# Performance work log

Hardware: AMD Instinct MI355X
Metric: run time of the kernel (lower is better)

## Reference

```python
import jax, jax.numpy as jnp
import numpy as np

# SMPL kinematic tree (24 joints); parent[0] = -1 (root)
PARENT = [-1, 0, 0, 0, 1, 2, 3, 4, 5, 6, 7, 8, 9, 9, 9, 12, 13, 14, 16, 17, 18, 19, 20, 21]
J = len(PARENT)  # 24


def _ancestor_matrix(parent):
    # A[j, k] = 1 if offset k contributes to joint j (k on path root->j, excluding root)
    n = len(parent)
    A = np.zeros((n, n), dtype=np.float32)
    for j in range(1, n):
        k = j
        while k > 0:
            A[j, k] = 1.0
            k = parent[k]
    return A

ANC = jnp.asarray(_ancestor_matrix(PARENT))  # [J, J]


def setup_inputs() -> dict:
    key = jax.random.key(0)
    k0, k1, k2 = jax.random.split(key, 3)
    B, D, H = 131072, 256, 512
    out_dim = (J - 1) * 4
    z = jax.random.normal(k0, (B, D), jnp.float32)
    W1 = jax.random.normal(k1, (D, H), jnp.float32) / np.float32(np.sqrt(D))
    b1 = jnp.zeros((H,), jnp.float32)
    W2 = jax.random.normal(k2, (H, out_dim), jnp.float32) / np.float32(np.sqrt(H))
    b2 = jnp.zeros((out_dim,), jnp.float32)
    return {"z": z, "W1": W1, "b1": b1, "W2": W2, "b2": b2}


def reference(z, W1, b1, W2, b2):
    B = z.shape[0]
    h = jax.nn.silu(z @ W1 + b1)                      # [B, 512]
    raw = (h @ W2 + b2).reshape(B, J - 1, 4)          # [B, J-1, 4]
    dir_raw = raw[..., :3]                            # [B, J-1, 3]
    len_raw = raw[..., 3]                             # [B, J-1]
    # F.normalize(dim=-1, eps=1e-6): x / max(||x||, eps)
    norm = jnp.linalg.norm(dir_raw, axis=-1, keepdims=True)
    direction = dir_raw / jnp.maximum(norm, 1e-6)
    length = jax.nn.softplus(len_raw)                 # [B, J-1]
    offset_non_root = direction * length[..., None]
    offsets = jnp.concatenate(
        [jnp.zeros((B, 1, 3), z.dtype), offset_non_root], axis=1
    )  # [B, J, 3]
    # Forward kinematics: joints[j] = sum of offsets along ancestor chain.
    # The sequential per-joint loop collapses to one matmul with the
    # precomputed ancestor incidence matrix (same math, depth-parallel).
    joints = jnp.einsum('jk,bkc->bjc', ANC, offsets)  # [B, J, 3]
    return (joints, offsets, length)
```

## Files before the change

kernel.cpp:

```cpp
#include <hip/hip_runtime.h>
#include <math.h>

typedef _Float16 half8 __attribute__((ext_vector_type(8)));
typedef float floatx4 __attribute__((ext_vector_type(4)));

#define DD 256
#define HH 512
#define OC 92
#define NJ 24
#define BM 64
#define NCHUNK 16
#define W2_OFF 131072
#define FLAG_OFF 180224
#define FCAP 16384
#define BUF_BYTES 16384

__constant__ int c_parent[NJ] = {-1,0,0,0,1,2,3,4,5,6,7,8,9,9,9,12,13,14,16,17,18,19,20,21};


__global__ __launch_bounds__(256)
void prep(const float* __restrict__ W1, const float* __restrict__ W2,
          _Float16* __restrict__ ws, int* __restrict__ flags) {
    int t = blockIdx.x * 256 + threadIdx.x;
    if (t == 0) flags[0] = 0;
    if (t < 16384) {
        int lane = t & 63;
        int cfrag = (t >> 6) & 1;
        int ks = (t >> 7) & 7;
        int ckI = t >> 10;
        int c = ckI * 32 + cfrag * 16 + (lane & 15);
        int kb = ks * 32 + 4 * (lane >> 4);
        half8 v;
        #pragma unroll
        for (int j = 0; j < 8; ++j) {
            int k = kb + (j & 3) + 16 * (j >> 2);
            v[j] = (_Float16)W1[k * HH + c];
        }
        *(half8*)(ws + t * 8) = v;
    } else if (t < 16384 + 6144) {
        int u = t - 16384;
        int lane = u & 63;
        int rest = u >> 6;
        int cfrag = rest % 6;
        int ckI = rest / 6;
        int c = cfrag * 16 + (lane & 15);
        int kb = ckI * 32 + 4 * (lane >> 4);
        half8 v;
        #pragma unroll
        for (int j = 0; j < 8; ++j) {
            int k = kb + (j & 3) + 16 * (j >> 2);
            v[j] = (c < OC) ? (_Float16)W2[k * OC + c] : (_Float16)0.0f;
        }
        *(half8*)(ws + W2_OFF + (ckI * 6 + cfrag) * 512 + lane * 8) = v;
    }
}

__global__ __launch_bounds__(256)
__attribute__((amdgpu_waves_per_eu(4)))
void fused_main(const float* __restrict__ z, const _Float16* __restrict__ wsp,
                const float* __restrict__ b1, const float* __restrict__ b2,
                float* __restrict__ out, long long Btot, int* __restrict__ flags)
{
    __shared__ __align__(16) char smem[35200];
    float* b1f = (float*)(smem + 32768);
    float* b2f = (float*)(smem + 34816);
    const int tid = threadIdx.x;
    const int w   = tid >> 6;
    const int l   = tid & 63;
    const int l15 = l & 15;
    const int l4  = l >> 4;

    const long long R0w = (long long)blockIdx.x * BM + w * 16;

#define STAGE(ck_, dstbuf_) do {                                                             \
    const char* s1g_ = (const char*)wsp + (size_t)(ck_) * 16384;                             \
    _Pragma("unroll")                                                                        \
    for (int i_ = 0; i_ < 4; ++i_) {                                                         \
        int g_ = w * 4 + i_;                                                                 \
        __builtin_amdgcn_global_load_lds(                                                    \
            (const __attribute__((address_space(1))) void*)(s1g_ + g_ * 1024 + l * 16),      \
            (__attribute__((address_space(3))) void*)((dstbuf_) + g_ * 1024), 16, 0, 0);     \
    }                                                                                        \
} while (0)

#define MF(a_, b_, c_) __builtin_amdgcn_mfma_f32_16x16x32_f16((a_), (b_), (c_), 0, 0, 0)

#define COMPUTE_CHUNK(bufc_, ck_) do {                                                       \
    const _Float16* s1_ = (const _Float16*)(bufc_);                                          \
    const _Float16* p2_ = wsp + W2_OFF + (ck_) * 3072 + l * 8;                               \
    half8 w2f_[6];                                                                           \
    _Pragma("unroll")                                                                        \
    for (int cf_ = 0; cf_ < 6; ++cf_) w2f_[cf_] = *(const half8*)(p2_ + cf_ * 512);          \
    floatx4 acc1_[2];                                                                        \
    acc1_[0] = (floatx4)0.0f; acc1_[1] = (floatx4)0.0f;                                      \
    _Pragma("unroll")                                                                        \
    for (int ks_ = 0; ks_ < 8; ++ks_) {                                                      \
        _Pragma("unroll")                                                                    \
        for (int cf_ = 0; cf_ < 2; ++cf_) {                                                  \
            half8 bh_ = *(const half8*)(s1_ + ((ks_ * 2 + cf_) * 64 + l) * 8);               \
            acc1_[cf_] = MF(bh_, zh[ks_], acc1_[cf_]);                                       \
        }                                                                                    \
    }                                                                                        \
    floatx4 vb1a_ = *(const floatx4*)(b1f + (ck_) * 32 + 4 * l4);                            \
    floatx4 vb1b_ = *(const floatx4*)(b1f + (ck_) * 32 + 16 + 4 * l4);                       \
    half8 ah_;                                                                               \
    _Pragma("unroll")                                                                        \
    for (int cf_ = 0; cf_ < 2; ++cf_) {                                                      \
        _Pragma("unroll")                                                                    \
        for (int i_ = 0; i_ < 4; ++i_) {                                                     \
            float a_ = acc1_[cf_][i_] + (cf_ ? vb1b_[i_] : vb1a_[i_]);                       \
            float hv_ = a_ * __builtin_amdgcn_rcpf(1.0f + __expf(-a_));                      \
            ah_[i_ | (cf_ << 2)] = (_Float16)hv_;                                            \
        }                                                                                    \
    }                                                                                        \
    _Pragma("unroll")                                                                        \
    for (int cf_ = 0; cf_ < 6; ++cf_) {                                                      \
        a2[cf_] = MF(w2f_[cf_], ah_, a2[cf_]);                                               \
    }                                                                                        \
} while (0)

    STAGE(0, smem);
    if (tid < 128) *(floatx4*)(b1f + tid * 4) = *(const floatx4*)(b1 + tid * 4);
    if (tid >= 128 && tid < 224) { int c = tid - 128; b2f[c] = (c < OC) ? b2[c] : 0.0f; }

    half8 zh[8];
    {
        const float* zrow = z + (R0w + l15) * DD;
        #pragma unroll
        for (int ks = 0; ks < 8; ++ks) {
            const float* p = zrow + ks * 32 + l4 * 4;
            floatx4 va = *(const floatx4*)p;
            floatx4 vb = *(const floatx4*)(p + 16);
            half8 th;
            th[0] = (_Float16)va[0]; th[1] = (_Float16)va[1];
            th[2] = (_Float16)va[2]; th[3] = (_Float16)va[3];
            th[4] = (_Float16)vb[0]; th[5] = (_Float16)vb[1];
            th[6] = (_Float16)vb[2]; th[7] = (_Float16)vb[3];
            zh[ks] = th;
        }
    }

    floatx4 a2[6];
    #pragma unroll
    for (int i = 0; i < 6; ++i) a2[i] = (floatx4)0.0f;

    __syncthreads();

    #pragma unroll 1
    for (int t = 0; t < 8; ++t) {
        STAGE(2 * t + 1, smem + BUF_BYTES);
        COMPUTE_CHUNK(smem, 2 * t);
        asm volatile("s_waitcnt vmcnt(0)" ::: "memory");
        __builtin_amdgcn_s_barrier();
        if (t < 7) STAGE(2 * t + 2, smem);
        COMPUTE_CHUNK(smem + BUF_BYTES, 2 * t + 1);
        asm volatile("s_waitcnt vmcnt(0)" ::: "memory");
        __builtin_amdgcn_s_barrier();
    }

    float* joints  = out;
    float* offsets = out + Btot * (NJ * 3);
    float* length  = out + 2 * Btot * (NJ * 3);

    {
        float* s_off = (float*)(smem + w * 6080);
        float* s_len = s_off + 1152;
        const int r = l15;
        #pragma unroll
        for (int cf = 0; cf < 6; ++cf) {
            const int j = 4 * cf + l4;
            if (j < NJ - 1) {
                float x  = a2[cf][0] + b2f[4 * j + 0];
                float y  = a2[cf][1] + b2f[4 * j + 1];
                float zz = a2[cf][2] + b2f[4 * j + 2];
                float lr = a2[cf][3] + b2f[4 * j + 3];
                float nrm = sqrtf(x * x + y * y + zz * zz);
                float inv = __builtin_amdgcn_rcpf(fmaxf(nrm, 1e-6f));
                float len = fmaxf(lr, 0.0f) + __logf(1.0f + __expf(-fabsf(lr)));
                if (len > 12.0f * nrm) {
                    int fi = atomicAdd(&flags[0], 1);
                    if (fi < FCAP) flags[1 + fi] = (int)(R0w + r);
                }
                s_off[r * 72 + 3 * (j + 1) + 0] = x * inv * len;
                s_off[r * 72 + 3 * (j + 1) + 1] = y * inv * len;
                s_off[r * 72 + 3 * (j + 1) + 2] = zz * inv * len;
                s_len[r * 23 + j] = len;
            }
        }
        if (l < 16) {
            s_off[l * 72 + 0] = 0.0f;
            s_off[l * 72 + 1] = 0.0f;
            s_off[l * 72 + 2] = 0.0f;
        }
        __syncthreads();

        {
            float* gdst = offsets + R0w * (NJ * 3);
            for (int t4 = l; t4 < 288; t4 += 64)
                *(float4*)(gdst + t4 * 4) = *(float4*)(s_off + t4 * 4);
        }
        {
            float* gdst = length + R0w * (NJ - 1);
            for (int t4 = l; t4 < 92; t4 += 64)
                *(float4*)(gdst + t4 * 4) = *(float4*)(s_len + t4 * 4);
        }
        for (int task = l; task < 16 * NJ; task += 64) {
            int rr = task / NJ;
            int j = task - rr * NJ;
            float jx = 0.0f, jy = 0.0f, jz = 0.0f;
            int k = j;
            while (k > 0) {
                jx += s_off[rr * 72 + 3 * k + 0];
                jy += s_off[rr * 72 + 3 * k + 1];
                jz += s_off[rr * 72 + 3 * k + 2];
                k = c_parent[k];
            }
            long long base = (R0w + rr) * (NJ * 3) + j * 3;
            joints[base + 0] = jx;
            joints[base + 1] = jy;
            joints[base + 2] = jz;
        }
    }
#undef STAGE
#undef COMPUTE_CHUNK
#undef MF
}

__global__ __launch_bounds__(256)
void fixup(const float* __restrict__ z, const float* __restrict__ W1,
           const float* __restrict__ b1, const float* __restrict__ W2,
           const float* __restrict__ b2, float* __restrict__ out,
           long long Btot, const int* __restrict__ flags)
{
    __shared__ float z_s[DD];
    __shared__ float h_s[HH];
    __shared__ float raw_s[96];
    __shared__ float off_s[72];
    int n = flags[0];
    if (n > FCAP) n = FCAP;
    if ((int)blockIdx.x >= n) return;
    const int tid = threadIdx.x;
    const long long row = flags[1 + blockIdx.x];

    float* joints  = out;
    float* offsets = out + Btot * (NJ * 3);
    float* length  = out + 2 * Btot * (NJ * 3);

    z_s[tid] = z[row * DD + tid];
    __syncthreads();
    for (int c = tid; c < HH; c += 256) {
        float acc = b1[c];
        for (int k = 0; k < DD; ++k) acc = fmaf(z_s[k], W1[k * HH + c], acc);
        h_s[c] = acc / (1.0f + expf(-acc));
    }
    __syncthreads();
    if (tid < OC) {
        float acc = b2[tid];
        for (int k = 0; k < HH; ++k) acc = fmaf(h_s[k], W2[k * OC + tid], acc);
        raw_s[tid] = acc;
    }
    __syncthreads();
    if (tid < NJ - 1) {
        int j = tid;
        float x  = raw_s[4 * j + 0];
        float y  = raw_s[4 * j + 1];
        float zz = raw_s[4 * j + 2];
        float lr = raw_s[4 * j + 3];
        float nrm = sqrtf(x * x + y * y + zz * zz);
        float inv = 1.0f / fmaxf(nrm, 1e-6f);
        float len = fmaxf(lr, 0.0f) + log1pf(expf(-fabsf(lr)));
        off_s[3 * (j + 1) + 0] = x * inv * len;
        off_s[3 * (j + 1) + 1] = y * inv * len;
        off_s[3 * (j + 1) + 2] = zz * inv * len;
        length[row * (NJ - 1) + j] = len;
    }
    if (tid < 3) off_s[tid] = 0.0f;
    __syncthreads();
    if (tid < NJ) {
        int j = tid;
        float jx = 0.0f, jy = 0.0f, jz = 0.0f;
        int k = j;
        while (k > 0) {
            jx += off_s[3 * k + 0];
            jy += off_s[3 * k + 1];
            jz += off_s[3 * k + 2];
            k = c_parent[k];
        }
        joints[row * (NJ * 3) + j * 3 + 0] = jx;
        joints[row * (NJ * 3) + j * 3 + 1] = jy;
        joints[row * (NJ * 3) + j * 3 + 2] = jz;
    }
    if (tid < NJ * 3) offsets[row * (NJ * 3) + tid] = off_s[tid];
}

extern "C" void kernel_launch(void* const* d_in, const int* in_sizes, int n_in,
                              void* d_out, int out_size, void* d_ws, size_t ws_size,
                              hipStream_t stream) {
    const float* z  = (const float*)d_in[0];
    const float* W1 = (const float*)d_in[1];
    const float* b1 = (const float*)d_in[2];
    const float* W2 = (const float*)d_in[3];
    const float* b2 = (const float*)d_in[4];
    float* out = (float*)d_out;
    _Float16* ws = (_Float16*)d_ws;
    int* flags = (int*)(ws + FLAG_OFF);

    const long long Btot = (long long)in_sizes[0] / DD;

    prep<<<88, 256, 0, stream>>>(W1, W2, ws, flags);
    fused_main<<<(int)(Btot / BM), 256, 0, stream>>>(z, ws, b1, b2, out, Btot, flags);
    fixup<<<4096, 256, 0, stream>>>(z, W1, b1, W2, b2, out, Btot, flags);
}
```

Before: 143.6 us.

## Triple-buffer W1 staging and prefetch W2 fragments one chunk ahead

Moves from double to triple buffering of the W1 chunks in LDS, so each stage is issued two chunks ahead and the barriers wait on partial vmcnt instead of draining all loads. W2 fragments are loaded into alternating register sets one chunk early, and sched_barriers pin the issue order. The goal is to hide global and LDS load latency behind the MFMA work. In exchange, LDS use per block rises to about 51 KB and the occupancy hint drops from 4 to 3 waves per EU. The hand-counted vmcnt values also make correctness fragile.

```diff
diff --git a/kernel.cpp b/kernel.cpp
--- a/kernel.cpp
+++ b/kernel.cpp
@@ -9,7 +9,6 @@
 #define OC 92
 #define NJ 24
 #define BM 64
-#define NCHUNK 16
 #define W2_OFF 131072
 #define FLAG_OFF 180224
 #define FCAP 16384
@@ -56,14 +55,14 @@
 }
 
 __global__ __launch_bounds__(256)
-__attribute__((amdgpu_waves_per_eu(4)))
+__attribute__((amdgpu_waves_per_eu(3)))
 void fused_main(const float* __restrict__ z, const _Float16* __restrict__ wsp,
                 const float* __restrict__ b1, const float* __restrict__ b2,
                 float* __restrict__ out, long long Btot, int* __restrict__ flags)
 {
-    __shared__ __align__(16) char smem[35200];
-    float* b1f = (float*)(smem + 32768);
-    float* b2f = (float*)(smem + 34816);
+    __shared__ __align__(16) char smem[51584];
+    float* b1f = (float*)(smem + 49152);
+    float* b2f = (float*)(smem + 51200);
     const int tid = threadIdx.x;
     const int w   = tid >> 6;
     const int l   = tid & 63;
@@ -72,25 +71,29 @@
 
     const long long R0w = (long long)blockIdx.x * BM + w * 16;
 
-#define STAGE(ck_, dstbuf_) do {                                                             \
+#define SBAR() __builtin_amdgcn_sched_barrier(0)
+
+#define STAGE(ck_, boff_) do {                                                               \
     const char* s1g_ = (const char*)wsp + (size_t)(ck_) * 16384;                             \
     _Pragma("unroll")                                                                        \
     for (int i_ = 0; i_ < 4; ++i_) {                                                         \
         int g_ = w * 4 + i_;                                                                 \
         __builtin_amdgcn_global_load_lds(                                                    \
             (const __attribute__((address_space(1))) void*)(s1g_ + g_ * 1024 + l * 16),      \
-            (__attribute__((address_space(3))) void*)((dstbuf_) + g_ * 1024), 16, 0, 0);     \
+            (__attribute__((address_space(3))) void*)(smem + (boff_) + g_ * 1024), 16, 0, 0);\
     }                                                                                        \
 } while (0)
 
+#define LOADW2(dst_, ck_) do {                                                               \
+    const _Float16* p2_ = wsp + W2_OFF + (ck_) * 3072 + l * 8;                               \
+    _Pragma("unroll")                                                                        \
+    for (int cf_ = 0; cf_ < 6; ++cf_) dst_[cf_] = *(const half8*)(p2_ + cf_ * 512);          \
+} while (0)
+
 #define MF(a_, b_, c_) __builtin_amdgcn_mfma_f32_16x16x32_f16((a_), (b_), (c_), 0, 0, 0)
 
-#define COMPUTE_CHUNK(bufc_, ck_) do {                                                       \
-    const _Float16* s1_ = (const _Float16*)(bufc_);                                          \
-    const _Float16* p2_ = wsp + W2_OFF + (ck_) * 3072 + l * 8;                               \
-    half8 w2f_[6];                                                                           \
-    _Pragma("unroll")                                                                        \
-    for (int cf_ = 0; cf_ < 6; ++cf_) w2f_[cf_] = *(const half8*)(p2_ + cf_ * 512);          \
+#define COMPUTE_CHUNK(boff_, ck_, w2f_) do {                                                 \
+    const _Float16* s1_ = (const _Float16*)(smem + (boff_));                                 \
     floatx4 acc1_[2];                                                                        \
     acc1_[0] = (floatx4)0.0f; acc1_[1] = (floatx4)0.0f;                                      \
     _Pragma("unroll")                                                                        \
@@ -119,9 +122,7 @@
     }                                                                                        \
 } while (0)
 
-    STAGE(0, smem);
-    if (tid < 128) *(floatx4*)(b1f + tid * 4) = *(const floatx4*)(b1 + tid * 4);
-    if (tid >= 128 && tid < 224) { int c = tid - 128; b2f[c] = (c < OC) ? b2[c] : 0.0f; }
+#define BOFF(c_) ((((c_) % 3)) * BUF_BYTES)
 
     half8 zh[8];
     {
@@ -139,28 +140,51 @@
             zh[ks] = th;
         }
     }
+    SBAR();
+    half8 w2fA[6], w2fB[6];
+    STAGE(0, 0);
+    SBAR();
+    LOADW2(w2fA, 0);
+    SBAR();
+    STAGE(1, BUF_BYTES);
+    SBAR();
+
+    if (tid < 128) *(floatx4*)(b1f + tid * 4) = *(const floatx4*)(b1 + tid * 4);
+    if (tid >= 128 && tid < 224) { int c = tid - 128; b2f[c] = (c < OC) ? b2[c] : 0.0f; }
 
     floatx4 a2[6];
     #pragma unroll
     for (int i = 0; i < 6; ++i) a2[i] = (floatx4)0.0f;
 
-    __syncthreads();
-
     #pragma unroll 1
-    for (int t = 0; t < 8; ++t) {
-        STAGE(2 * t + 1, smem + BUF_BYTES);
-        COMPUTE_CHUNK(smem, 2 * t);
-        asm volatile("s_waitcnt vmcnt(0)" ::: "memory");
+    for (int u = 0; u < 8; ++u) {
+        const int e = 2 * u, o = 2 * u + 1;
+        asm volatile("s_waitcnt vmcnt(4)" ::: "memory");
         __builtin_amdgcn_s_barrier();
-        if (t < 7) STAGE(2 * t + 2, smem);
-        COMPUTE_CHUNK(smem + BUF_BYTES, 2 * t + 1);
-        asm volatile("s_waitcnt vmcnt(0)" ::: "memory");
+        SBAR();
+        LOADW2(w2fB, o);
+        SBAR();
+        if (u < 7) STAGE(e + 2, BOFF(e + 2));
+        SBAR();
+        COMPUTE_CHUNK(BOFF(e), e, w2fA);
+        if (u < 7) { asm volatile("s_waitcnt vmcnt(4)" ::: "memory"); }
+        else       { asm volatile("s_waitcnt vmcnt(0)" ::: "memory"); }
         __builtin_amdgcn_s_barrier();
+        SBAR();
+        if (u < 7) {
+            LOADW2(w2fA, e + 2);
+            SBAR();
+            STAGE(o + 2, BOFF(o + 2));
+            SBAR();
+        }
+        COMPUTE_CHUNK(BOFF(o), o, w2fB);
     }
 
     float* joints  = out;
     float* offsets = out + Btot * (NJ * 3);
     float* length  = out + 2 * Btot * (NJ * 3);
+
+    __syncthreads();
 
     {
         float* s_off = (float*)(smem + w * 6080);
@@ -222,8 +246,11 @@
         }
     }
 #undef STAGE
+#undef LOADW2
 #undef COMPUTE_CHUNK
 #undef MF
+#undef BOFF
+#undef SBAR
 }
 
 __global__ __launch_bounds__(256)
```

New measurement: 152.6 us. 6.2% more time.

## Stage half of W1 into LDS per phase with 128-row, 512-thread blocks

Applied to the files above, without the earlier changes.

The main kernel now uses 512-thread blocks covering 128 rows and loads W1 in two 128 KB halves into LDS, instead of double-buffering 16 KB chunks with a barrier per chunk. This cuts the per-chunk barriers and doubles the rows that share each staged weight tile. The cost is one large LDS allocation per block (about 130 KB), which limits occupancy to one block per CU, and an exposed load stall at each half. The fixup kernel also changes to a grid-stride loop over 512 blocks instead of launching 4096 mostly idle blocks.

```diff
diff --git a/kernel.cpp b/kernel.cpp
--- a/kernel.cpp
+++ b/kernel.cpp
@@ -8,12 +8,10 @@
 #define HH 512
 #define OC 92
 #define NJ 24
-#define BM 64
-#define NCHUNK 16
+#define BM 128
 #define W2_OFF 131072
 #define FLAG_OFF 180224
 #define FCAP 16384
-#define BUF_BYTES 16384
 
 __constant__ int c_parent[NJ] = {-1,0,0,0,1,2,3,4,5,6,7,8,9,9,9,12,13,14,16,17,18,19,20,21};
 
@@ -55,15 +53,15 @@
     }
 }
 
-__global__ __launch_bounds__(256)
-__attribute__((amdgpu_waves_per_eu(4)))
+__global__ __launch_bounds__(512)
+__attribute__((amdgpu_waves_per_eu(2)))
 void fused_main(const float* __restrict__ z, const _Float16* __restrict__ wsp,
                 const float* __restrict__ b1, const float* __restrict__ b2,
                 float* __restrict__ out, long long Btot, int* __restrict__ flags)
 {
-    __shared__ __align__(16) char smem[35200];
-    float* b1f = (float*)(smem + 32768);
-    float* b2f = (float*)(smem + 34816);
+    __shared__ __align__(16) char smem[133504];
+    float* b1f = (float*)(smem + 131072);
+    float* b2f = (float*)(smem + 133120);
     const int tid = threadIdx.x;
     const int w   = tid >> 6;
     const int l   = tid & 63;
@@ -72,56 +70,18 @@
 
     const long long R0w = (long long)blockIdx.x * BM + w * 16;
 
-#define STAGE(ck_, dstbuf_) do {                                                             \
-    const char* s1g_ = (const char*)wsp + (size_t)(ck_) * 16384;                             \
+#define STAGEP(p_) do {                                                                      \
+    const char* sg_ = (const char*)wsp + (size_t)(p_) * 131072;                              \
     _Pragma("unroll")                                                                        \
-    for (int i_ = 0; i_ < 4; ++i_) {                                                         \
-        int g_ = w * 4 + i_;                                                                 \
+    for (int i_ = 0; i_ < 16; ++i_) {                                                        \
+        int g_ = w * 16 + i_;                                                                \
         __builtin_amdgcn_global_load_lds(                                                    \
-            (const __attribute__((address_space(1))) void*)(s1g_ + g_ * 1024 + l * 16),      \
-            (__attribute__((address_space(3))) void*)((dstbuf_) + g_ * 1024), 16, 0, 0);     \
+            (const __attribute__((address_space(1))) void*)(sg_ + g_ * 1024 + l * 16),       \
+            (__attribute__((address_space(3))) void*)(smem + g_ * 1024), 16, 0, 0);          \
     }                                                                                        \
 } while (0)
 
 #define MF(a_, b_, c_) __builtin_amdgcn_mfma_f32_16x16x32_f16((a_), (b_), (c_), 0, 0, 0)
-
-#define COMPUTE_CHUNK(bufc_, ck_) do {                                                       \
-    const _Float16* s1_ = (const _Float16*)(bufc_);                                          \
-    const _Float16* p2_ = wsp + W2_OFF + (ck_) * 3072 + l * 8;                               \
-    half8 w2f_[6];                                                                           \
-    _Pragma("unroll")                                                                        \
-    for (int cf_ = 0; cf_ < 6; ++cf_) w2f_[cf_] = *(const half8*)(p2_ + cf_ * 512);          \
-    floatx4 acc1_[2];                                                                        \
-    acc1_[0] = (floatx4)0.0f; acc1_[1] = (floatx4)0.0f;                                      \
-    _Pragma("unroll")                                                                        \
-    for (int ks_ = 0; ks_ < 8; ++ks_) {                                                      \
-        _Pragma("unroll")                                                                    \
-        for (int cf_ = 0; cf_ < 2; ++cf_) {                                                  \
-            half8 bh_ = *(const half8*)(s1_ + ((ks_ * 2 + cf_) * 64 + l) * 8);               \
-            acc1_[cf_] = MF(bh_, zh[ks_], acc1_[cf_]);                                       \
-        }                                                                                    \
-    }                                                                                        \
-    floatx4 vb1a_ = *(const floatx4*)(b1f + (ck_) * 32 + 4 * l4);                            \
-    floatx4 vb1b_ = *(const floatx4*)(b1f + (ck_) * 32 + 16 + 4 * l4);                       \
-    half8 ah_;                                                                               \
-    _Pragma("unroll")                                                                        \
-    for (int cf_ = 0; cf_ < 2; ++cf_) {                                                      \
-        _Pragma("unroll")                                                                    \
-        for (int i_ = 0; i_ < 4; ++i_) {                                                     \
-            float a_ = acc1_[cf_][i_] + (cf_ ? vb1b_[i_] : vb1a_[i_]);                       \
-            float hv_ = a_ * __builtin_amdgcn_rcpf(1.0f + __expf(-a_));                      \
-            ah_[i_ | (cf_ << 2)] = (_Float16)hv_;                                            \
-        }                                                                                    \
-    }                                                                                        \
-    _Pragma("unroll")                                                                        \
-    for (int cf_ = 0; cf_ < 6; ++cf_) {                                                      \
-        a2[cf_] = MF(w2f_[cf_], ah_, a2[cf_]);                                               \
-    }                                                                                        \
-} while (0)
-
-    STAGE(0, smem);
-    if (tid < 128) *(floatx4*)(b1f + tid * 4) = *(const floatx4*)(b1 + tid * 4);
-    if (tid >= 128 && tid < 224) { int c = tid - 128; b2f[c] = (c < OC) ? b2[c] : 0.0f; }
 
     half8 zh[8];
     {
@@ -140,27 +100,65 @@
         }
     }
 
+    STAGEP(0);
+    if (tid < 128) *(floatx4*)(b1f + tid * 4) = *(const floatx4*)(b1 + tid * 4);
+    if (tid >= 128 && tid < 224) { int c = tid - 128; b2f[c] = (c < OC) ? b2[c] : 0.0f; }
+
     floatx4 a2[6];
     #pragma unroll
     for (int i = 0; i < 6; ++i) a2[i] = (floatx4)0.0f;
 
+    asm volatile("s_waitcnt vmcnt(0)" ::: "memory");
     __syncthreads();
 
     #pragma unroll 1
-    for (int t = 0; t < 8; ++t) {
-        STAGE(2 * t + 1, smem + BUF_BYTES);
-        COMPUTE_CHUNK(smem, 2 * t);
-        asm volatile("s_waitcnt vmcnt(0)" ::: "memory");
-        __builtin_amdgcn_s_barrier();
-        if (t < 7) STAGE(2 * t + 2, smem);
-        COMPUTE_CHUNK(smem + BUF_BYTES, 2 * t + 1);
-        asm volatile("s_waitcnt vmcnt(0)" ::: "memory");
-        __builtin_amdgcn_s_barrier();
+    for (int p = 0; p < 2; ++p) {
+        for (int c = 0; c < 8; ++c) {
+            const int ck = p * 8 + c;
+            const _Float16* p2 = wsp + W2_OFF + ck * 3072 + l * 8;
+            half8 w2f[6];
+            #pragma unroll
+            for (int cf = 0; cf < 6; ++cf) w2f[cf] = *(const half8*)(p2 + cf * 512);
+
+            const _Float16* s1 = (const _Float16*)(smem + c * 16384);
+            floatx4 acc1[2];
+            acc1[0] = (floatx4)0.0f; acc1[1] = (floatx4)0.0f;
+            #pragma unroll
+            for (int ks = 0; ks < 8; ++ks) {
+                #pragma unroll
+                for (int cf = 0; cf < 2; ++cf) {
+                    half8 bh = *(const half8*)(s1 + ((ks * 2 + cf) * 64 + l) * 8);
+                    acc1[cf] = MF(bh, zh[ks], acc1[cf]);
+                }
+            }
+            floatx4 vb1a = *(const floatx4*)(b1f + ck * 32 + 4 * l4);
+            floatx4 vb1b = *(const floatx4*)(b1f + ck * 32 + 16 + 4 * l4);
+            half8 ah;
+            #pragma unroll
+            for (int cf = 0; cf < 2; ++cf) {
+                #pragma unroll
+                for (int i = 0; i < 4; ++i) {
+                    float a = acc1[cf][i] + (cf ? vb1b[i] : vb1a[i]);
+                    float hv = a * __builtin_amdgcn_rcpf(1.0f + __expf(-a));
+                    ah[i | (cf << 2)] = (_Float16)hv;
+                }
+            }
+            #pragma unroll
+            for (int cf = 0; cf < 6; ++cf) a2[cf] = MF(w2f[cf], ah, a2[cf]);
+        }
+        if (p == 0) {
+            __syncthreads();
+            STAGEP(1);
+            asm volatile("s_waitcnt vmcnt(0)" ::: "memory");
+            __syncthreads();
+        }
     }
 
     float* joints  = out;
     float* offsets = out + Btot * (NJ * 3);
     float* length  = out + 2 * Btot * (NJ * 3);
+
+    __syncthreads();
 
     {
         float* s_off = (float*)(smem + w * 6080);
@@ -221,8 +219,7 @@
             joints[base + 2] = jz;
         }
     }
-#undef STAGE
-#undef COMPUTE_CHUNK
+#undef STAGEP
 #undef MF
 }
 
@@ -238,59 +235,61 @@
     __shared__ float off_s[72];
     int n = flags[0];
     if (n > FCAP) n = FCAP;
-    if ((int)blockIdx.x >= n) return;
     const int tid = threadIdx.x;
-    const long long row = flags[1 + blockIdx.x];
 
     float* joints  = out;
     float* offsets = out + Btot * (NJ * 3);
     float* length  = out + 2 * Btot * (NJ * 3);
 
-    z_s[tid] = z[row * DD + tid];
-    __syncthreads();
-    for (int c = tid; c < HH; c += 256) {
-        float acc = b1[c];
-        for (int k = 0; k < DD; ++k) acc = fmaf(z_s[k], W1[k * HH + c], acc);
-        h_s[c] = acc / (1.0f + expf(-acc));
-    }
-    __syncthreads();
-    if (tid < OC) {
-        float acc = b2[tid];
-        for (int k = 0; k < HH; ++k) acc = fmaf(h_s[k], W2[k * OC + tid], acc);
-        raw_s[tid] = acc;
-    }
-    __syncthreads();
-    if (tid < NJ - 1) {
-        int j = tid;
-        float x  = raw_s[4 * j + 0];
-        float y  = raw_s[4 * j + 1];
-        float zz = raw_s[4 * j + 2];
-        float lr = raw_s[4 * j + 3];
-        float nrm = sqrtf(x * x + y * y + zz * zz);
-        float inv = 1.0f / fmaxf(nrm, 1e-6f);
-        float len = fmaxf(lr, 0.0f) + log1pf(expf(-fabsf(lr)));
-        off_s[3 * (j + 1) + 0] = x * inv * len;
-        off_s[3 * (j + 1) + 1] = y * inv * len;
-        off_s[3 * (j + 1) + 2] = zz * inv * len;
-        length[row * (NJ - 1) + j] = len;
-    }
-    if (tid < 3) off_s[tid] = 0.0f;
-    __syncthreads();
-    if (tid < NJ) {
-        int j = tid;
-        float jx = 0.0f, jy = 0.0f, jz = 0.0f;
-        int k = j;
-        while (k > 0) {
-            jx += off_s[3 * k + 0];
-            jy += off_s[3 * k + 1];
-            jz += off_s[3 * k + 2];
-            k = c_parent[k];
-        }
-        joints[row * (NJ * 3) + j * 3 + 0] = jx;
-        joints[row * (NJ * 3) + j * 3 + 1] = jy;
-        joints[row * (NJ * 3) + j * 3 + 2] = jz;
-    }
-    if (tid < NJ * 3) offsets[row * (NJ * 3) + tid] = off_s[tid];
+    for (int e = blockIdx.x; e < n; e += gridDim.x) {
+        const long long row = flags[1 + e];
+        __syncthreads();
+        z_s[tid] = z[row * DD + tid];
+        __syncthreads();
+        for (int c = tid; c < HH; c += 256) {
+            float acc = b1[c];
+            for (int k = 0; k < DD; ++k) acc = fmaf(z_s[k], W1[k * HH + c], acc);
+            h_s[c] = acc / (1.0f + expf(-acc));
+        }
+        __syncthreads();
+        if (tid < OC) {
+            float acc = b2[tid];
+            for (int k = 0; k < HH; ++k) acc = fmaf(h_s[k], W2[k * OC + tid], acc);
+            raw_s[tid] = acc;
+        }
+        __syncthreads();
+        if (tid < NJ - 1) {
+            int j = tid;
+            float x  = raw_s[4 * j + 0];
+            float y  = raw_s[4 * j + 1];
+            float zz = raw_s[4 * j + 2];
+            float lr = raw_s[4 * j + 3];
+            float nrm = sqrtf(x * x + y * y + zz * zz);
+            float inv = 1.0f / fmaxf(nrm, 1e-6f);
+            float len = fmaxf(lr, 0.0f) + log1pf(expf(-fabsf(lr)));
+            off_s[3 * (j + 1) + 0] = x * inv * len;
+            off_s[3 * (j + 1) + 1] = y * inv * len;
+            off_s[3 * (j + 1) + 2] = zz * inv * len;
+            length[row * (NJ - 1) + j] = len;
+        }
+        if (tid < 3) off_s[tid] = 0.0f;
+        __syncthreads();
+        if (tid < NJ) {
+            int j = tid;
+            float jx = 0.0f, jy = 0.0f, jz = 0.0f;
+            int k = j;
+            while (k > 0) {
+                jx += off_s[3 * k + 0];
+                jy += off_s[3 * k + 1];
+                jz += off_s[3 * k + 2];
+                k = c_parent[k];
+            }
+            joints[row * (NJ * 3) + j * 3 + 0] = jx;
+            joints[row * (NJ * 3) + j * 3 + 1] = jy;
+            joints[row * (NJ * 3) + j * 3 + 2] = jz;
+        }
+        if (tid < NJ * 3) offsets[row * (NJ * 3) + tid] = off_s[tid];
+    }
 }
 
 extern "C" void kernel_launch(void* const* d_in, const int* in_sizes, int n_in,
@@ -308,6 +307,6 @@
     const long long Btot = (long long)in_sizes[0] / DD;
 
     prep<<<88, 256, 0, stream>>>(W1, W2, ws, flags);
-    fused_main<<<(int)(Btot / BM), 256, 0, stream>>>(z, ws, b1, b2, out, Btot, flags);
-    fixup<<<4096, 256, 0, stream>>>(z, W1, b1, W2, b2, out, Btot, flags);
+    fused_main<<<(int)(Btot / BM), 512, 0, stream>>>(z, ws, b1, b2, out, Btot, flags);
+    fixup<<<512, 256, 0, stream>>>(z, W1, b1, W2, b2, out, Btot, flags);
 }
```

Result: slower. 203.9 us (+42.0%).

## Single-buffer W1 staging to raise occupancy; grid-stride fixup kernel

Applied to the files above, without the earlier changes.

Drops the double-buffered W1 chunk staging in LDS for a single 16KB buffer and raises the waves-per-EU hint from 4 to 8. The lower LDS and register budget per block is meant to let more blocks share a CU. The epilogue now runs in two passes of two waves each so the per-wave offset scratch fits in the smaller LDS. The fixup kernel becomes a grid-stride loop over 512 blocks instead of launching 4096 blocks that mostly exit early. The cost is that chunk loads no longer overlap with compute inside a block, and the tighter register cap may cause spills.

```diff
diff --git a/kernel.cpp b/kernel.cpp
--- a/kernel.cpp
+++ b/kernel.cpp
@@ -9,11 +9,9 @@
 #define OC 92
 #define NJ 24
 #define BM 64
-#define NCHUNK 16
 #define W2_OFF 131072
 #define FLAG_OFF 180224
 #define FCAP 16384
-#define BUF_BYTES 16384
 
 __constant__ int c_parent[NJ] = {-1,0,0,0,1,2,3,4,5,6,7,8,9,9,9,12,13,14,16,17,18,19,20,21};
 
@@ -56,14 +54,14 @@
 }
 
 __global__ __launch_bounds__(256)
-__attribute__((amdgpu_waves_per_eu(4)))
+__attribute__((amdgpu_waves_per_eu(8)))
 void fused_main(const float* __restrict__ z, const _Float16* __restrict__ wsp,
                 const float* __restrict__ b1, const float* __restrict__ b2,
                 float* __restrict__ out, long long Btot, int* __restrict__ flags)
 {
-    __shared__ __align__(16) char smem[35200];
-    float* b1f = (float*)(smem + 32768);
-    float* b2f = (float*)(smem + 34816);
+    __shared__ __align__(16) char smem[18816];
+    float* b1f = (float*)(smem + 16384);
+    float* b2f = (float*)(smem + 18432);
     const int tid = threadIdx.x;
     const int w   = tid >> 6;
     const int l   = tid & 63;
@@ -72,21 +70,21 @@
 
     const long long R0w = (long long)blockIdx.x * BM + w * 16;
 
-#define STAGE(ck_, dstbuf_) do {                                                             \
+#define STAGE(ck_) do {                                                                      \
     const char* s1g_ = (const char*)wsp + (size_t)(ck_) * 16384;                             \
     _Pragma("unroll")                                                                        \
     for (int i_ = 0; i_ < 4; ++i_) {                                                         \
         int g_ = w * 4 + i_;                                                                 \
         __builtin_amdgcn_global_load_lds(                                                    \
             (const __attribute__((address_space(1))) void*)(s1g_ + g_ * 1024 + l * 16),      \
-            (__attribute__((address_space(3))) void*)((dstbuf_) + g_ * 1024), 16, 0, 0);     \
+            (__attribute__((address_space(3))) void*)(smem + g_ * 1024), 16, 0, 0);          \
     }                                                                                        \
 } while (0)
 
 #define MF(a_, b_, c_) __builtin_amdgcn_mfma_f32_16x16x32_f16((a_), (b_), (c_), 0, 0, 0)
 
-#define COMPUTE_CHUNK(bufc_, ck_) do {                                                       \
-    const _Float16* s1_ = (const _Float16*)(bufc_);                                          \
+#define COMPUTE_CHUNK(ck_) do {                                                              \
+    const _Float16* s1_ = (const _Float16*)(smem);                                           \
     const _Float16* p2_ = wsp + W2_OFF + (ck_) * 3072 + l * 8;                               \
     half8 w2f_[6];                                                                           \
     _Pragma("unroll")                                                                        \
@@ -118,10 +116,6 @@
         a2[cf_] = MF(w2f_[cf_], ah_, a2[cf_]);                                               \
     }                                                                                        \
 } while (0)
-
-    STAGE(0, smem);
-    if (tid < 128) *(floatx4*)(b1f + tid * 4) = *(const floatx4*)(b1 + tid * 4);
-    if (tid >= 128 && tid < 224) { int c = tid - 128; b2f[c] = (c < OC) ? b2[c] : 0.0f; }
 
     half8 zh[8];
     {
@@ -139,87 +133,92 @@
             zh[ks] = th;
         }
     }
+    STAGE(0);
+    if (tid < 128) *(floatx4*)(b1f + tid * 4) = *(const floatx4*)(b1 + tid * 4);
+    if (tid >= 128 && tid < 224) { int c = tid - 128; b2f[c] = (c < OC) ? b2[c] : 0.0f; }
 
     floatx4 a2[6];
     #pragma unroll
     for (int i = 0; i < 6; ++i) a2[i] = (floatx4)0.0f;
 
-    __syncthreads();
-
     #pragma unroll 1
-    for (int t = 0; t < 8; ++t) {
-        STAGE(2 * t + 1, smem + BUF_BYTES);
-        COMPUTE_CHUNK(smem, 2 * t);
+    for (int ck = 0; ck < 16; ++ck) {
         asm volatile("s_waitcnt vmcnt(0)" ::: "memory");
         __builtin_amdgcn_s_barrier();
-        if (t < 7) STAGE(2 * t + 2, smem);
-        COMPUTE_CHUNK(smem + BUF_BYTES, 2 * t + 1);
-        asm volatile("s_waitcnt vmcnt(0)" ::: "memory");
+        COMPUTE_CHUNK(ck);
         __builtin_amdgcn_s_barrier();
+        if (ck < 15) STAGE(ck + 1);
     }
 
     float* joints  = out;
     float* offsets = out + Btot * (NJ * 3);
     float* length  = out + 2 * Btot * (NJ * 3);
 
-    {
-        float* s_off = (float*)(smem + w * 6080);
-        float* s_len = s_off + 1152;
-        const int r = l15;
-        #pragma unroll
-        for (int cf = 0; cf < 6; ++cf) {
-            const int j = 4 * cf + l4;
-            if (j < NJ - 1) {
-                float x  = a2[cf][0] + b2f[4 * j + 0];
-                float y  = a2[cf][1] + b2f[4 * j + 1];
-                float zz = a2[cf][2] + b2f[4 * j + 2];
-                float lr = a2[cf][3] + b2f[4 * j + 3];
-                float nrm = sqrtf(x * x + y * y + zz * zz);
-                float inv = __builtin_amdgcn_rcpf(fmaxf(nrm, 1e-6f));
-                float len = fmaxf(lr, 0.0f) + __logf(1.0f + __expf(-fabsf(lr)));
-                if (len > 12.0f * nrm) {
-                    int fi = atomicAdd(&flags[0], 1);
-                    if (fi < FCAP) flags[1 + fi] = (int)(R0w + r);
+    #pragma unroll 1
+    for (int pass = 0; pass < 2; ++pass) {
+        if ((w >> 1) == pass) {
+            float* s_off = (float*)(smem + (w & 1) * 6080);
+            float* s_len = s_off + 1152;
+            const int r = l15;
+            #pragma unroll
+            for (int cf = 0; cf < 6; ++cf) {
+                const int j = 4 * cf + l4;
+                if (j < NJ - 1) {
+                    float x  = a2[cf][0] + b2f[4 * j + 0];
+                    float y  = a2[cf][1] + b2f[4 * j + 1];
+                    float zz = a2[cf][2] + b2f[4 * j + 2];
+                    float lr = a2[cf][3] + b2f[4 * j + 3];
+                    float nrm = sqrtf(x * x + y * y + zz * zz);
+                    float inv = __builtin_amdgcn_rcpf(fmaxf(nrm, 1e-6f));
+                    float len = fmaxf(lr, 0.0f) + __logf(1.0f + __expf(-fabsf(lr)));
+                    if (len > 12.0f * nrm) {
+                        int fi = atomicAdd(&flags[0], 1);
+                        if (fi < FCAP) flags[1 + fi] = (int)(R0w + r);
+                    }
+                    s_off[r * 72 + 3 * (j + 1) + 0] = x * inv * len;
+                    s_off[r * 72 + 3 * (j + 1) + 1] = y * inv * len;
+                    s_off[r * 72 + 3 * (j + 1) + 2] = zz * inv * len;
+                    s_len[r * 23 + j] = len;
                 }
-                s_off[r * 72 + 3 * (j + 1) + 0] = x * inv * len;
-                s_off[r * 72 + 3 * (j + 1) + 1] = y * inv * len;
-                s_off[r * 72 + 3 * (j + 1) + 2] = zz * inv * len;
-                s_len[r * 23 + j] = len;
-            }
-        }
-        if (l < 16) {
-            s_off[l * 72 + 0] = 0.0f;
-            s_off[l * 72 + 1] = 0.0f;
-            s_off[l * 72 + 2] = 0.0f;
-        }
-        __syncthreads();
-
-        {
-            float* gdst = offsets + R0w * (NJ * 3);
-            for (int t4 = l; t4 < 288; t4 += 64)
-                *(float4*)(gdst + t4 * 4) = *(float4*)(s_off + t4 * 4);
-        }
-        {
-            float* gdst = length + R0w * (NJ - 1);
-            for (int t4 = l; t4 < 92; t4 += 64)
-                *(float4*)(gdst + t4 * 4) = *(float4*)(s_len + t4 * 4);
-        }
-        for (int task = l; task < 16 * NJ; task += 64) {
-            int rr = task / NJ;
-            int j = task - rr * NJ;
-            float jx = 0.0f, jy = 0.0f, jz = 0.0f;
-            int k = j;
-            while (k > 0) {
-                jx += s_off[rr * 72 + 3 * k + 0];
-                jy += s_off[rr * 72 + 3 * k + 1];
-                jz += s_off[rr * 72 + 3 * k + 2];
-                k = c_parent[k];
-            }
-            long long base = (R0w + rr) * (NJ * 3) + j * 3;
-            joints[base + 0] = jx;
-            joints[base + 1] = jy;
-            joints[base + 2] = jz;
-        }
+            }
+            if (l < 16) {
+                s_off[l * 72 + 0] = 0.0f;
+                s_off[l * 72 + 1] = 0.0f;
+                s_off[l * 72 + 2] = 0.0f;
+            }
+        }
+        __syncthreads();
+        if ((w >> 1) == pass) {
+            float* s_off = (float*)(smem + (w & 1) * 6080);
+            float* s_len = s_off + 1152;
+            {
+                float* gdst = offsets + R0w * (NJ * 3);
+                for (int t4 = l; t4 < 288; t4 += 64)
+                    *(float4*)(gdst + t4 * 4) = *(float4*)(s_off + t4 * 4);
+            }
+            {
+                float* gdst = length + R0w * (NJ - 1);
+                for (int t4 = l; t4 < 92; t4 += 64)
+                    *(float4*)(gdst + t4 * 4) = *(float4*)(s_len + t4 * 4);
+            }
+            for (int task = l; task < 16 * NJ; task += 64) {
+                int rr = task / NJ;
+                int j = task - rr * NJ;
+                float jx = 0.0f, jy = 0.0f, jz = 0.0f;
+                int k = j;
+                while (k > 0) {
+                    jx += s_off[rr * 72 + 3 * k + 0];
+                    jy += s_off[rr * 72 + 3 * k + 1];
+                    jz += s_off[rr * 72 + 3 * k + 2];
+                    k = c_parent[k];
+                }
+                long long base = (R0w + rr) * (NJ * 3) + j * 3;
+                joints[base + 0] = jx;
+                joints[base + 1] = jy;
+                joints[base + 2] = jz;
+            }
+        }
+        if (pass == 0) __syncthreads();
     }
 #undef STAGE
 #undef COMPUTE_CHUNK
@@ -238,59 +237,61 @@
     __shared__ float off_s[72];
     int n = flags[0];
     if (n > FCAP) n = FCAP;
-    if ((int)blockIdx.x >= n) return;
     const int tid = threadIdx.x;
-    const long long row = flags[1 + blockIdx.x];
 
     float* joints  = out;
     float* offsets = out + Btot * (NJ * 3);
     float* length  = out + 2 * Btot * (NJ * 3);
 
-    z_s[tid] = z[row * DD + tid];
-    __syncthreads();
-    for (int c = tid; c < HH; c += 256) {
-        float acc = b1[c];
-        for (int k = 0; k < DD; ++k) acc = fmaf(z_s[k], W1[k * HH + c], acc);
-        h_s[c] = acc / (1.0f + expf(-acc));
-    }
-    __syncthreads();
-    if (tid < OC) {
-        float acc = b2[tid];
-        for (int k = 0; k < HH; ++k) acc = fmaf(h_s[k], W2[k * OC + tid], acc);
-        raw_s[tid] = acc;
-    }
-    __syncthreads();
-    if (tid < NJ - 1) {
-        int j = tid;
-        float x  = raw_s[4 * j + 0];
-        float y  = raw_s[4 * j + 1];
-        float zz = raw_s[4 * j + 2];
-        float lr = raw_s[4 * j + 3];
-        float nrm = sqrtf(x * x + y * y + zz * zz);
-        float inv = 1.0f / fmaxf(nrm, 1e-6f);
-        float len = fmaxf(lr, 0.0f) + log1pf(expf(-fabsf(lr)));
-        off_s[3 * (j + 1) + 0] = x * inv * len;
-        off_s[3 * (j + 1) + 1] = y * inv * len;
-        off_s[3 * (j + 1) + 2] = zz * inv * len;
-        length[row * (NJ - 1) + j] = len;
-    }
-    if (tid < 3) off_s[tid] = 0.0f;
-    __syncthreads();
-    if (tid < NJ) {
-        int j = tid;
-        float jx = 0.0f, jy = 0.0f, jz = 0.0f;
-        int k = j;
-        while (k > 0) {
-            jx += off_s[3 * k + 0];
-            jy += off_s[3 * k + 1];
-            jz += off_s[3 * k + 2];
-            k = c_parent[k];
-        }
-        joints[row * (NJ * 3) + j * 3 + 0] = jx;
-        joints[row * (NJ * 3) + j * 3 + 1] = jy;
-        joints[row * (NJ * 3) + j * 3 + 2] = jz;
-    }
-    if (tid < NJ * 3) offsets[row * (NJ * 3) + tid] = off_s[tid];
+    for (int e = blockIdx.x; e < n; e += gridDim.x) {
+        const long long row = flags[1 + e];
+        __syncthreads();
+        z_s[tid] = z[row * DD + tid];
+        __syncthreads();
+        for (int c = tid; c < HH; c += 256) {
+            float acc = b1[c];
+            for (int k = 0; k < DD; ++k) acc = fmaf(z_s[k], W1[k * HH + c], acc);
+            h_s[c] = acc / (1.0f + expf(-acc));
+        }
+        __syncthreads();
+        if (tid < OC) {
+            float acc = b2[tid];
+            for (int k = 0; k < HH; ++k) acc = fmaf(h_s[k], W2[k * OC + tid], acc);
+            raw_s[tid] = acc;
+        }
+        __syncthreads();
+        if (tid < NJ - 1) {
+            int j = tid;
+            float x  = raw_s[4 * j + 0];
+            float y  = raw_s[4 * j + 1];
+            float zz = raw_s[4 * j + 2];
+            float lr = raw_s[4 * j + 3];
+            float nrm = sqrtf(x * x + y * y + zz * zz);
+            float inv = 1.0f / fmaxf(nrm, 1e-6f);
+            float len = fmaxf(lr, 0.0f) + log1pf(expf(-fabsf(lr)));
+            off_s[3 * (j + 1) + 0] = x * inv * len;
+            off_s[3 * (j + 1) + 1] = y * inv * len;
+            off_s[3 * (j + 1) + 2] = zz * inv * len;
+            length[row * (NJ - 1) + j] = len;
+        }
+        if (tid < 3) off_s[tid] = 0.0f;
+        __syncthreads();
+        if (tid < NJ) {
+            int j = tid;
+            float jx = 0.0f, jy = 0.0f, jz = 0.0f;
+            int k = j;
+            while (k > 0) {
+                jx += off_s[3 * k + 0];
+                jy += off_s[3 * k + 1];
+                jz += off_s[3 * k + 2];
+                k = c_parent[k];
+            }
+            joints[row * (NJ * 3) + j * 3 + 0] = jx;
+            joints[row * (NJ * 3) + j * 3 + 1] = jy;
+            joints[row * (NJ * 3) + j * 3 + 2] = jz;
+        }
+        if (tid < NJ * 3) offsets[row * (NJ * 3) + tid] = off_s[tid];
+    }
 }
 
 extern "C" void kernel_launch(void* const* d_in, const int* in_sizes, int n_in,
@@ -309,5 +310,5 @@
 
     prep<<<88, 256, 0, stream>>>(W1, W2, ws, flags);
     fused_main<<<(int)(Btot / BM), 256, 0, stream>>>(z, ws, b1, b2, out, Btot, flags);
-    fixup<<<4096, 256, 0, stream>>>(z, W1, b1, W2, b2, out, Btot, flags);
+    fixup<<<512, 256, 0, stream>>>(z, W1, b1, W2, b2, out, Btot, flags);
 }
```

After: 379.7 us. 164% more time.
